# Kernel optimization log

Measured on AMD Instinct MI355X. Metric: run time of the kernel, lower is better.

Reference implementation:

```python
import jax, jax.numpy as jnp
import numpy as np

Q_NODES = 100000
S_NODES = 100000
N_EDGES = 3200000
D = 3
HIDDEN = 64
OUT_DIM = 128
STAT_DIM = 3 + 2 * D  # N_i, D_avg, D_var, Delta(D), PCA(D)


def setup_inputs() -> dict:
    key = jax.random.key(0)
    ks = jax.random.split(key, 7)
    source_pos = jax.random.normal(ks[0], (S_NODES, D), dtype=jnp.float32)
    query_pos = jax.random.normal(ks[1], (Q_NODES, D), dtype=jnp.float32)
    qi = jax.random.randint(ks[2], (N_EDGES,), 0, Q_NODES, dtype=jnp.int64)
    si = jax.random.randint(ks[3], (N_EDGES,), 0, S_NODES, dtype=jnp.int64)
    edge_index = jnp.stack([qi, si], axis=0)
    # MLP params (torch Linear default-ish scale)
    W1 = jax.random.normal(ks[4], (HIDDEN, STAT_DIM), dtype=jnp.float32) / np.sqrt(STAT_DIM)
    b1 = jnp.zeros((HIDDEN,), dtype=jnp.float32)
    W2 = jax.random.normal(ks[5], (OUT_DIM, HIDDEN), dtype=jnp.float32) / np.sqrt(HIDDEN)
    b2 = jnp.zeros((OUT_DIM,), dtype=jnp.float32)
    return {"source_pos": source_pos, "query_pos": query_pos, "edge_index": edge_index,
            "W1": W1, "b1": b1, "W2": W2, "b2": b2}


def _stat_features(source_pos, query_pos, edge_index):
    Q = query_pos.shape[0]
    qi = edge_index[0]
    si = edge_index[1]
    ones = jnp.ones(qi.shape, dtype=jnp.float32)
    counts = jax.ops.segment_sum(ones, qi, num_segments=Q)          # [Q] = N_i
    has = counts > 0
    Nc = jnp.where(has, counts, 1.0)                                 # clamp 0 -> 1

    nbr = source_pos[si]                                             # [E,D]
    qc = query_pos[qi]                                               # [E,D]
    dist = jnp.linalg.norm(nbr - qc, axis=1)                         # [E]
    D_avg = jax.ops.segment_sum(dist, qi, num_segments=Q) / Nc       # [Q]
    E_X2 = jax.ops.segment_sum(dist * dist, qi, num_segments=Q) / Nc
    D_var = jnp.maximum(E_X2 - D_avg * D_avg, 0.0)

    centroid = jax.ops.segment_sum(nbr, qi, num_segments=Q) / Nc[:, None]  # [Q,D]
    Delta = centroid - query_pos                                     # [Q,D]

    centered = nbr - centroid[qi]                                    # [E,D]
    cov_comp = centered[:, :, None] * centered[:, None, :]           # [E,D,D]
    cov = jax.ops.segment_sum(cov_comp, qi, num_segments=Q) / Nc[:, None, None]

    eig = jnp.linalg.eigvalsh(cov)[:, ::-1]                          # descending [Q,D]
    PCA = jnp.where(has[:, None], eig, 0.0)

    feats = jnp.concatenate([counts[:, None], D_avg[:, None], D_var[:, None], Delta, PCA], axis=1)
    feats = jnp.where(has[:, None], feats, 0.0)

    mean = feats.mean(axis=0, keepdims=True)
    std = jnp.std(feats, axis=0, ddof=1, keepdims=True)              # torch std is unbiased
    std = jnp.where(std < 1e-6, 1.0, std)
    return (feats - mean) / std


def reference(source_pos, query_pos, edge_index, W1, b1, W2, b2):
    feats = _stat_features(source_pos, query_pos, edge_index)        # [Q, 9]
    h = jax.nn.relu(feats @ W1.T + b1)
    return h @ W2.T + b2                                             # [Q, OUT_DIM]
```

## Files before the change

### kernel.cpp

```cpp
#include <hip/hip_runtime.h>
#include <math.h>

#define Q_NODES 100000
#define S_NODES 100000
#define N_EDGES 3200000
#define HIDDEN 64
#define OUT_DIM 128

#define QPB   128
#define NB    782
#define CAPB  4608
#define TILE  4096
#define NT4   (N_EDGES / 4)

#define F_CURSOR_OFF 0
#define F_NORM_OFF   3200
#define F_PSUM_OFF   3328
#define F_PSUMSQ_OFF 31488
#define F_FEATS_OFF  59648
#define F_SP4_OFF    3659648
#define F_SLOTS_OFF  5259648
#define F_ZERO_BYTES 3200
#define F_WS_NEED    (5259648ull + (unsigned long long)(NB * CAPB + 1) * 4)

#define B_ACC_OFF    0
#define B_STATS_OFF  4800000
#define B_NORM_OFF   4800144
#define B_FEATS_OFF  4800224
#define B_ZERO_BYTES 4800144

__device__ __forceinline__ void atomAddF(float* p, float v) {
#if defined(__gfx950__) || defined(__gfx942__) || defined(__gfx90a__)
    unsafeAtomicAdd(p, v);
#else
    atomicAdd(p, v);
#endif
}


__device__ __forceinline__ void eig3_sym(
        float a00, float a01, float a02, float a11, float a12, float a22,
        float& e1, float& e2, float& e3) {
    float p1 = a01 * a01 + a02 * a02 + a12 * a12;
    float qm = (a00 + a11 + a22) * (1.0f / 3.0f);
    float b00 = a00 - qm, b11 = a11 - qm, b22 = a22 - qm;
    float p2 = b00 * b00 + b11 * b11 + b22 * b22 + 2.0f * p1;
    if (p2 <= 1e-24f) {
        e1 = qm; e2 = qm; e3 = qm;
    } else {
        float p = sqrtf(p2 * (1.0f / 6.0f));
        float invp = 1.0f / p;
        float c00 = b00 * invp, c11 = b11 * invp, c22 = b22 * invp;
        float c01 = a01 * invp, c02 = a02 * invp, c12 = a12 * invp;
        float detB = c00 * (c11 * c22 - c12 * c12)
                   - c01 * (c01 * c22 - c12 * c02)
                   + c02 * (c01 * c12 - c11 * c02);
        float r = 0.5f * detB;
        r = fminf(fmaxf(r, -1.0f), 1.0f);
        float phi = acosf(r) * (1.0f / 3.0f);
        e1 = qm + 2.0f * p * cosf(phi);
        e3 = qm + 2.0f * p * cosf(phi + 2.0943951023931953f);
        e2 = 3.0f * qm - e1 - e3;
    }
}

__device__ __forceinline__ void sums_to_feats(
        const float* s, float qx, float qy, float qz, float* f) {
    float n = s[0];
#pragma unroll
    for (int k = 0; k < 9; ++k) f[k] = 0.0f;
    if (n > 0.0f) {
        float inv = 1.0f / n;
        float Davg = s[1] * inv;
        float Dvar = fmaxf(s[2] * inv - Davg * Davg, 0.0f);
        float cx = s[3] * inv, cy = s[4] * inv, cz = s[5] * inv;
        float a00 = fmaxf(s[6] * inv - cx * cx, 0.0f);
        float a01 = s[7] * inv - cx * cy;
        float a02 = s[8] * inv - cx * cz;
        float a11 = fmaxf(s[9] * inv - cy * cy, 0.0f);
        float a12 = s[10] * inv - cy * cz;
        float a22 = fmaxf(s[11] * inv - cz * cz, 0.0f);
        float e1, e2, e3;
        eig3_sym(a00, a01, a02, a11, a12, a22, e1, e2, e3);
        f[0] = n; f[1] = Davg; f[2] = Dvar;
        f[3] = cx - qx; f[4] = cy - qy; f[5] = cz - qz;
        f[6] = e1; f[7] = e2; f[8] = e3;
    }
}


__global__ __launch_bounds__(512, 4) void partition_kernel(
        const int* __restrict__ edge,
        const float* __restrict__ sp,
        float4* __restrict__ sp4,
        int* __restrict__ cursor,
        unsigned int* __restrict__ slots) {
    __shared__ unsigned int s_rec[TILE];
    __shared__ int s_posh[TILE];
    __shared__ int s_cur[NB];
    __shared__ int s_off[NB];
    __shared__ int s_wsum[8];

    int tid = threadIdx.x;
    int lane = tid & 63, wv = tid >> 6;
    int tileStart = blockIdx.x * TILE;
    int tileCount = N_EDGES - tileStart;
    if (tileCount > TILE) tileCount = TILE;

    {
        int i = blockIdx.x * 512 + tid;
        if (i < S_NODES)
            sp4[i] = make_float4(sp[3 * i], sp[3 * i + 1], sp[3 * i + 2], 0.0f);
    }

    for (int b = tid; b < NB; b += 512) s_posh[b] = 0;
    __syncthreads();

    const int4* eq4 = (const int4*)edge;
    const int4* es4 = (const int4*)(edge + N_EDGES);
    int base4 = blockIdx.x * (TILE / 4);
    int4 q4[2], s4[2];
    bool v[2];
#pragma unroll
    for (int j = 0; j < 2; ++j) {
        int i4 = base4 + tid + j * 512;
        v[j] = i4 < NT4;
        int ic = v[j] ? i4 : 0;
        q4[j] = eq4[ic];
        s4[j] = es4[ic];
        if (v[j]) {
            atomicAdd(&s_posh[q4[j].x >> 7], 1);
            atomicAdd(&s_posh[q4[j].y >> 7], 1);
            atomicAdd(&s_posh[q4[j].z >> 7], 1);
            atomicAdd(&s_posh[q4[j].w >> 7], 1);
        }
    }
    __syncthreads();

    int local[4], tsum = 0;
#pragma unroll
    for (int j = 0; j < 4; ++j) {
        int idx = 4 * tid + j;
        local[j] = (idx < NB) ? s_posh[idx] : 0;
        tsum += local[j];
    }
    int inc = tsum;
#pragma unroll
    for (int off = 1; off < 64; off <<= 1) {
        int t = __shfl_up(inc, off);
        if (lane >= off) inc += t;
    }
    if (lane == 63) s_wsum[wv] = inc;
    __syncthreads();
    int wbase = 0;
    for (int w = 0; w < wv; ++w) wbase += s_wsum[w];
    int run = wbase + inc - tsum;
#pragma unroll
    for (int j = 0; j < 4; ++j) {
        int idx = 4 * tid + j;
        if (idx < NB) s_cur[idx] = run;
        run += local[j];
    }
    __syncthreads();

    for (int b = tid; b < NB; b += 512) {
        int c = s_posh[b];
        int base = c ? atomicAdd(&cursor[b], c) : 0;
        s_off[b] = b * CAPB + base - s_cur[b];
    }
    __syncthreads();

#pragma unroll
    for (int j = 0; j < 2; ++j) {
        if (v[j]) {
            int qs[4] = { q4[j].x, q4[j].y, q4[j].z, q4[j].w };
            int ss[4] = { s4[j].x, s4[j].y, s4[j].z, s4[j].w };
#pragma unroll
            for (int m = 0; m < 4; ++m) {
                int bkt = qs[m] >> 7;
                int idx = atomicAdd(&s_cur[bkt], 1);
                int gpos = idx + s_off[bkt];
                if (gpos >= (bkt + 1) * CAPB) gpos = NB * CAPB;
                s_rec[idx] = ((unsigned)(qs[m] & (QPB - 1)) << 17) | (unsigned)ss[m];
                s_posh[idx] = gpos;
            }
        }
    }
    __syncthreads();

    for (int i = tid; i < tileCount; i += 512)
        slots[s_posh[i]] = s_rec[i];
}

__global__ __launch_bounds__(512) void bucket_kernel(
        const int* __restrict__ cursor,
        const unsigned int* __restrict__ slots,
        const float4* __restrict__ sp4,
        const float* __restrict__ qp,
        float* __restrict__ feats,
        float* __restrict__ psum,
        float* __restrict__ psumsq) {
    __shared__ unsigned int s_sorted[CAPB];
    __shared__ float qtile[QPB * 3];
    __shared__ int s_cnt[QPB], s_start[QPB], s_cur[QPB];
    __shared__ float s_part[4][QPB][13];
    __shared__ float s_red1[8][9], s_red2[8][9];

    int tid = threadIdx.x;
    int b = blockIdx.x;
    int cnt = cursor[b];
    if (cnt > CAPB) cnt = CAPB;

    if (tid < QPB) s_cnt[tid] = 0;
    for (int i = tid; i < QPB * 3; i += 512) {
        int g = b * QPB * 3 + i;
        qtile[i] = (g < Q_NODES * 3) ? qp[g] : 0.0f;
    }
    __syncthreads();

    const unsigned int* bslots = slots + b * CAPB;
    for (int i = tid; i < cnt; i += 512)
        atomicAdd(&s_cnt[bslots[i] >> 17], 1);
    __syncthreads();

    if (tid < 64) {
        int a0 = s_cnt[tid], a1 = s_cnt[64 + tid];
        int i0 = a0, i1 = a1;
#pragma unroll
        for (int off = 1; off < 64; off <<= 1) {
            int t0 = __shfl_up(i0, off); if (tid >= off) i0 += t0;
            int t1 = __shfl_up(i1, off); if (tid >= off) i1 += t1;
        }
        int tot0 = __shfl(i0, 63);
        s_start[tid] = i0 - a0;              s_cur[tid] = i0 - a0;
        s_start[64 + tid] = i1 - a1 + tot0;  s_cur[64 + tid] = i1 - a1 + tot0;
    }
    __syncthreads();

    for (int i = tid; i < cnt; i += 512) {
        unsigned rec = bslots[i];
        int pos = atomicAdd(&s_cur[rec >> 17], 1);
        s_sorted[pos] = rec;
    }
    __syncthreads();

    {
        int q = tid & (QPB - 1);
        int sub = tid >> 7;
        float qx = qtile[3 * q + 0], qy = qtile[3 * q + 1], qz = qtile[3 * q + 2];
        float s[12];
#pragma unroll
        for (int k = 0; k < 12; ++k) s[k] = 0.0f;
        int st = s_start[q], deg = s_cnt[q];
        for (int j = sub; j < deg; j += 4) {
            unsigned rec = s_sorted[st + j];
            float4 sv = sp4[rec & 0x1FFFF];
            float dx = sv.x - qx, dy = sv.y - qy, dz = sv.z - qz;
            float d2 = dx * dx + dy * dy + dz * dz;
            s[0] += 1.0f;
            s[1] += sqrtf(d2);
            s[2] += d2;
            s[3] += sv.x; s[4] += sv.y; s[5] += sv.z;
            s[6] += sv.x * sv.x; s[7] += sv.x * sv.y; s[8] += sv.x * sv.z;
            s[9] += sv.y * sv.y; s[10] += sv.y * sv.z; s[11] += sv.z * sv.z;
        }
#pragma unroll
        for (int k = 0; k < 12; ++k) s_part[sub][q][k] = s[k];
    }
    __syncthreads();

    float f[9];
#pragma unroll
    for (int k = 0; k < 9; ++k) f[k] = 0.0f;
    int q = b * QPB + (tid & (QPB - 1));
    if (tid < QPB && q < Q_NODES) {
        float qx = qtile[3 * tid + 0], qy = qtile[3 * tid + 1], qz = qtile[3 * tid + 2];
        float s[12];
#pragma unroll
        for (int k = 0; k < 12; ++k)
            s[k] = ((s_part[0][tid][k] + s_part[1][tid][k])
                  + (s_part[2][tid][k] + s_part[3][tid][k]));
        sums_to_feats(s, qx, qy, qz, f);
#pragma unroll
        for (int k = 0; k < 9; ++k) feats[k * Q_NODES + q] = f[k];
    }

    int lane = tid & 63, wv = tid >> 6;
#pragma unroll
    for (int k = 0; k < 9; ++k) {
        float s1 = f[k];
        float s2 = f[k] * f[k];
#pragma unroll
        for (int off = 32; off > 0; off >>= 1) {
            s1 += __shfl_down(s1, off);
            s2 += __shfl_down(s2, off);
        }
        if (lane == 0) { s_red1[wv][k] = s1; s_red2[wv][k] = s2; }
    }
    __syncthreads();
    if (tid < 9) {
        float t1 = 0.0f, t2 = 0.0f;
#pragma unroll
        for (int w = 0; w < 8; ++w) { t1 += s_red1[w][tid]; t2 += s_red2[w][tid]; }
        psum[tid * NB + b]   = t1;
        psumsq[tid * NB + b] = t2;
    }
}

__global__ __launch_bounds__(576) void stats_reduce_kernel(
        const float* __restrict__ psum,
        const float* __restrict__ psumsq,
        float* __restrict__ norm) {
    int k = threadIdx.x >> 6, lane = threadIdx.x & 63;
    if (k >= 9) return;
    double a1 = 0.0, a2 = 0.0;
    for (int b = lane; b < NB; b += 64) {
        a1 += (double)psum[k * NB + b];
        a2 += (double)psumsq[k * NB + b];
    }
#pragma unroll
    for (int off = 32; off > 0; off >>= 1) {
        a1 += __shfl_down(a1, off);
        a2 += __shfl_down(a2, off);
    }
    if (lane == 0) {
        double S = a1, S2 = a2;
        double mean = S / (double)Q_NODES;
        double var = (S2 - S * S / (double)Q_NODES) / (double)(Q_NODES - 1);
        if (var < 0.0) var = 0.0;
        double sd = sqrt(var);
        if (sd < 1e-6) sd = 1.0;
        norm[k] = (float)mean;
        norm[9 + k] = (float)(1.0 / sd);
    }
}


__global__ __launch_bounds__(256, 3) void mlp_kernel(
        const float* __restrict__ feats,
        const float* __restrict__ norm,
        const float* __restrict__ W1, const float* __restrict__ b1,
        const float* __restrict__ W2, const float* __restrict__ b2,
        float* __restrict__ out) {
    __shared__ float sW1[576];
    __shared__ float sB1[64];
    __shared__ float sB2[128];
    __shared__ float sNorm[18];
    __shared__ float w2t[64 * 64];
    __shared__ float ht[64 * 128];

    int tid = threadIdx.x;
    int blk_q = blockIdx.x;

    for (int i = tid; i < 576; i += 256) sW1[i] = W1[i];
    if (tid < 64) sB1[tid] = b1[tid];
    if (tid < 128) sB2[tid] = b2[tid];
    if (tid < 18) sNorm[tid] = norm[tid];

    {
        int o = tid & 63, kc = (tid >> 6) * 16;
#pragma unroll
        for (int j = 0; j < 16; ++j) {
            int k = kc + j;
            w2t[k * 64 + o] = W2[o * 64 + k];
        }
    }
    __syncthreads();

    {
        int q = tid & 127, half = tid >> 7;
        int qg = blk_q * 128 + q;
        int qc = qg < Q_NODES ? qg : Q_NODES - 1;
        float f[9];
#pragma unroll
        for (int k = 0; k < 9; ++k)
            f[k] = (feats[k * Q_NODES + qc] - sNorm[k]) * sNorm[9 + k];
#pragma unroll 4
        for (int j = 0; j < 32; ++j) {
            int ko = half * 32 + j;
            float a = sB1[ko];
#pragma unroll
            for (int kf = 0; kf < 9; ++kf) a = fmaf(f[kf], sW1[ko * 9 + kf], a);
            ht[ko * 128 + q] = fmaxf(a, 0.0f);
        }
    }
    __syncthreads();

    int qt = tid >> 4, ot = tid & 15;
    int q0 = qt * 8, o0 = ot * 4;

#pragma unroll 1
    for (int pass = 0; pass < 2; ++pass) {
        int oh = pass * 64;
        if (pass) {
            __syncthreads();
            int o = tid & 63, kc = (tid >> 6) * 16;
#pragma unroll
            for (int j = 0; j < 16; ++j) {
                int k = kc + j;
                w2t[k * 64 + o] = W2[(oh + o) * 64 + k];
            }
            __syncthreads();
        }

        float acc[8][4];
#pragma unroll
        for (int i = 0; i < 8; ++i)
#pragma unroll
            for (int j = 0; j < 4; ++j) acc[i][j] = 0.0f;

#pragma unroll 4
        for (int k = 0; k < 64; ++k) {
            float4 h0 = *(const float4*)&ht[k * 128 + q0];
            float4 h1 = *(const float4*)&ht[k * 128 + q0 + 4];
            float4 w  = *(const float4*)&w2t[k * 64 + o0];
            float hh[8] = { h0.x, h0.y, h0.z, h0.w, h1.x, h1.y, h1.z, h1.w };
#pragma unroll
            for (int i = 0; i < 8; ++i) {
                acc[i][0] = fmaf(hh[i], w.x, acc[i][0]);
                acc[i][1] = fmaf(hh[i], w.y, acc[i][1]);
                acc[i][2] = fmaf(hh[i], w.z, acc[i][2]);
                acc[i][3] = fmaf(hh[i], w.w, acc[i][3]);
            }
        }

        float4 bb = *(const float4*)&sB2[oh + o0];
#pragma unroll
        for (int i = 0; i < 8; ++i) {
            int qg = blk_q * 128 + q0 + i;
            if (qg < Q_NODES) {
                float4 vv = make_float4(acc[i][0] + bb.x, acc[i][1] + bb.y,
                                        acc[i][2] + bb.z, acc[i][3] + bb.w);
                *(float4*)(out + (size_t)qg * 128 + oh + o0) = vv;
            }
        }
    }
}


__global__ __launch_bounds__(256) void edge_kernel(
        const int* __restrict__ edge,
        const float* __restrict__ sp,
        const float* __restrict__ qp,
        float* __restrict__ acc) {
    int e = blockIdx.x * 256 + threadIdx.x;
    if (e >= N_EDGES) return;
    int q = edge[e];
    int s = edge[N_EDGES + e];
    float sx = sp[3 * s + 0], sy = sp[3 * s + 1], sz = sp[3 * s + 2];
    float qx = qp[3 * q + 0], qy = qp[3 * q + 1], qz = qp[3 * q + 2];
    float dx = sx - qx, dy = sy - qy, dz = sz - qz;
    float d2 = dx * dx + dy * dy + dz * dz;
    atomAddF(acc + 0 * Q_NODES + q, 1.0f);
    atomAddF(acc + 1 * Q_NODES + q, sqrtf(d2));
    atomAddF(acc + 2 * Q_NODES + q, d2);
    atomAddF(acc + 3 * Q_NODES + q, sx);
    atomAddF(acc + 4 * Q_NODES + q, sy);
    atomAddF(acc + 5 * Q_NODES + q, sz);
    atomAddF(acc + 6 * Q_NODES + q, sx * sx);
    atomAddF(acc + 7 * Q_NODES + q, sx * sy);
    atomAddF(acc + 8 * Q_NODES + q, sx * sz);
    atomAddF(acc + 9 * Q_NODES + q, sy * sy);
    atomAddF(acc + 10 * Q_NODES + q, sy * sz);
    atomAddF(acc + 11 * Q_NODES + q, sz * sz);
}

__global__ __launch_bounds__(256) void finalize_kernel(
        const float* __restrict__ acc,
        const float* __restrict__ qp,
        float* __restrict__ feats,
        double* __restrict__ stats) {
    int q = blockIdx.x * 256 + threadIdx.x;
    float f[9];
#pragma unroll
    for (int k = 0; k < 9; ++k) f[k] = 0.0f;
    if (q < Q_NODES) {
        float s[12];
#pragma unroll
        for (int k = 0; k < 12; ++k) s[k] = acc[k * Q_NODES + q];
        float qx = qp[3 * q + 0], qy = qp[3 * q + 1], qz = qp[3 * q + 2];
        sums_to_feats(s, qx, qy, qz, f);
#pragma unroll
        for (int k = 0; k < 9; ++k) feats[k * Q_NODES + q] = f[k];
    }
    int lane = threadIdx.x & 63;
#pragma unroll
    for (int k = 0; k < 9; ++k) {
        float s1 = f[k];
        float s2 = f[k] * f[k];
#pragma unroll
        for (int off = 32; off > 0; off >>= 1) {
            s1 += __shfl_down(s1, off);
            s2 += __shfl_down(s2, off);
        }
        if (lane == 0) {
            atomicAdd(&stats[k], (double)s1);
            atomicAdd(&stats[9 + k], (double)s2);
        }
    }
}

__global__ void stats_kernel(const double* __restrict__ stats,
                             float* __restrict__ norm) {
    int k = threadIdx.x;
    if (k < 9) {
        double S = stats[k], S2 = stats[9 + k];
        double mean = S / (double)Q_NODES;
        double var = (S2 - S * S / (double)Q_NODES) / (double)(Q_NODES - 1);
        if (var < 0.0) var = 0.0;
        double sd = sqrt(var);
        if (sd < 1e-6) sd = 1.0;
        norm[k] = (float)mean;
        norm[9 + k] = (float)(1.0 / sd);
    }
}


extern "C" void kernel_launch(void* const* d_in, const int* in_sizes, int n_in,
                              void* d_out, int out_size, void* d_ws, size_t ws_size,
                              hipStream_t stream) {
    const float* sp   = (const float*)d_in[0];
    const float* qp   = (const float*)d_in[1];
    const int*   edge = (const int*)d_in[2];
    const float* W1   = (const float*)d_in[3];
    const float* b1   = (const float*)d_in[4];
    const float* W2   = (const float*)d_in[5];
    const float* b2   = (const float*)d_in[6];
    float* out = (float*)d_out;
    char* ws = (char*)d_ws;

    if (ws_size >= F_WS_NEED) {
        int*          cursor = (int*)(ws + F_CURSOR_OFF);
        float*        norm   = (float*)(ws + F_NORM_OFF);
        float*        psum   = (float*)(ws + F_PSUM_OFF);
        float*        psumsq = (float*)(ws + F_PSUMSQ_OFF);
        float*        feats  = (float*)(ws + F_FEATS_OFF);
        float4*       sp4    = (float4*)(ws + F_SP4_OFF);
        unsigned int* slots  = (unsigned int*)(ws + F_SLOTS_OFF);

        hipMemsetAsync(ws, 0, F_ZERO_BYTES, stream);
        partition_kernel<<<(N_EDGES + TILE - 1) / TILE, 512, 0, stream>>>(
            edge, sp, sp4, cursor, slots);
        bucket_kernel<<<NB, 512, 0, stream>>>(cursor, slots, sp4, qp, feats, psum, psumsq);
        stats_reduce_kernel<<<1, 576, 0, stream>>>(psum, psumsq, norm);
        mlp_kernel<<<NB, 256, 0, stream>>>(feats, norm, W1, b1, W2, b2, out);
    } else {
        float*  acc   = (float*)(ws + B_ACC_OFF);
        double* stats = (double*)(ws + B_STATS_OFF);
        float*  norm  = (float*)(ws + B_NORM_OFF);
        float*  feats = (float*)(ws + B_FEATS_OFF);

        hipMemsetAsync(ws, 0, B_ZERO_BYTES, stream);
        edge_kernel<<<N_EDGES / 256, 256, 0, stream>>>(edge, sp, qp, acc);
        finalize_kernel<<<(Q_NODES + 255) / 256, 256, 0, stream>>>(acc, qp, feats, stats);
        stats_kernel<<<1, 64, 0, stream>>>(stats, norm);
        mlp_kernel<<<NB, 256, 0, stream>>>(feats, norm, W1, b1, W2, b2, out);
    }
}
```

Baseline: 193.1 us.

## Replace bucket counting sort with LDS atomics, fuse stats reduce, widen MLP

The per-bucket counting sort in LDS is removed. Each edge record now adds its 12 statistics straight into one of four replicated shared-memory accumulators using float atomics. The stats reduction is folded into the bucket kernel with a last-block-done counter, which drops one launch. Per-bucket cursors are padded to separate cache lines to cut atomic contention. The MLP now uses 512-thread blocks that stage features and the whole transposed W2 in LDS in a single pass. The trade-off is heavy LDS atomic traffic and nondeterministic summation order, in exchange for less sorting work and fewer launches.

```diff
diff --git a/kernel.cpp b/kernel.cpp
--- a/kernel.cpp
+++ b/kernel.cpp
@@ -12,16 +12,18 @@
 #define CAPB  4608
 #define TILE  4096
 #define NT4   (N_EDGES / 4)
+#define CSTR  16
 
 #define F_CURSOR_OFF 0
-#define F_NORM_OFF   3200
-#define F_PSUM_OFF   3328
-#define F_PSUMSQ_OFF 31488
-#define F_FEATS_OFF  59648
-#define F_SP4_OFF    3659648
-#define F_SLOTS_OFF  5259648
-#define F_ZERO_BYTES 3200
-#define F_WS_NEED    (5259648ull + (unsigned long long)(NB * CAPB + 1) * 4)
+#define F_DONE_OFF   50048
+#define F_NORM_OFF   50112
+#define F_PSUM_OFF   50240
+#define F_PSUMSQ_OFF 78400
+#define F_FEATS_OFF  106560
+#define F_SP4_OFF    3706560
+#define F_SLOTS_OFF  5306560
+#define F_ZERO_BYTES 50052
+#define F_WS_NEED    (5306560ull + (unsigned long long)(NB * CAPB + 1) * 4)
 
 #define B_ACC_OFF    0
 #define B_STATS_OFF  4800000
@@ -165,7 +167,7 @@
 
     for (int b = tid; b < NB; b += 512) {
         int c = s_posh[b];
-        int base = c ? atomicAdd(&cursor[b], c) : 0;
+        int base = c ? atomicAdd(&cursor[b * CSTR], c) : 0;
         s_off[b] = b * CAPB + base - s_cur[b];
     }
     __syncthreads();
@@ -192,80 +194,59 @@
         slots[s_posh[i]] = s_rec[i];
 }
 
-__global__ __launch_bounds__(512) void bucket_kernel(
+__global__ __launch_bounds__(512, 4) void bucket_kernel(
         const int* __restrict__ cursor,
         const unsigned int* __restrict__ slots,
         const float4* __restrict__ sp4,
         const float* __restrict__ qp,
         float* __restrict__ feats,
         float* __restrict__ psum,
-        float* __restrict__ psumsq) {
-    __shared__ unsigned int s_sorted[CAPB];
+        float* __restrict__ psumsq,
+        int* __restrict__ done,
+        float* __restrict__ norm) {
     __shared__ float qtile[QPB * 3];
-    __shared__ int s_cnt[QPB], s_start[QPB], s_cur[QPB];
     __shared__ float s_part[4][QPB][13];
     __shared__ float s_red1[8][9], s_red2[8][9];
+    __shared__ int s_last;
 
     int tid = threadIdx.x;
     int b = blockIdx.x;
-    int cnt = cursor[b];
+    int cnt = cursor[b * CSTR];
     if (cnt > CAPB) cnt = CAPB;
 
-    if (tid < QPB) s_cnt[tid] = 0;
     for (int i = tid; i < QPB * 3; i += 512) {
         int g = b * QPB * 3 + i;
         qtile[i] = (g < Q_NODES * 3) ? qp[g] : 0.0f;
     }
+    {
+        float* z = &s_part[0][0][0];
+        for (int i = tid; i < 4 * QPB * 13; i += 512) z[i] = 0.0f;
+    }
     __syncthreads();
 
     const unsigned int* bslots = slots + b * CAPB;
-    for (int i = tid; i < cnt; i += 512)
-        atomicAdd(&s_cnt[bslots[i] >> 17], 1);
-    __syncthreads();
-
-    if (tid < 64) {
-        int a0 = s_cnt[tid], a1 = s_cnt[64 + tid];
-        int i0 = a0, i1 = a1;
-#pragma unroll
-        for (int off = 1; off < 64; off <<= 1) {
-            int t0 = __shfl_up(i0, off); if (tid >= off) i0 += t0;
-            int t1 = __shfl_up(i1, off); if (tid >= off) i1 += t1;
-        }
-        int tot0 = __shfl(i0, 63);
-        s_start[tid] = i0 - a0;              s_cur[tid] = i0 - a0;
-        s_start[64 + tid] = i1 - a1 + tot0;  s_cur[64 + tid] = i1 - a1 + tot0;
-    }
-    __syncthreads();
-
+    int lane = tid & 63, wv = tid >> 6;
+    float* rep = &s_part[wv & 3][0][0];
     for (int i = tid; i < cnt; i += 512) {
         unsigned rec = bslots[i];
-        int pos = atomicAdd(&s_cur[rec >> 17], 1);
-        s_sorted[pos] = rec;
-    }
-    __syncthreads();
-
-    {
-        int q = tid & (QPB - 1);
-        int sub = tid >> 7;
+        int q = rec >> 17;
+        float4 sv = sp4[rec & 0x1FFFF];
         float qx = qtile[3 * q + 0], qy = qtile[3 * q + 1], qz = qtile[3 * q + 2];
-        float s[12];
-#pragma unroll
-        for (int k = 0; k < 12; ++k) s[k] = 0.0f;
-        int st = s_start[q], deg = s_cnt[q];
-        for (int j = sub; j < deg; j += 4) {
-            unsigned rec = s_sorted[st + j];
-            float4 sv = sp4[rec & 0x1FFFF];
-            float dx = sv.x - qx, dy = sv.y - qy, dz = sv.z - qz;
-            float d2 = dx * dx + dy * dy + dz * dz;
-            s[0] += 1.0f;
-            s[1] += sqrtf(d2);
-            s[2] += d2;
-            s[3] += sv.x; s[4] += sv.y; s[5] += sv.z;
-            s[6] += sv.x * sv.x; s[7] += sv.x * sv.y; s[8] += sv.x * sv.z;
-            s[9] += sv.y * sv.y; s[10] += sv.y * sv.z; s[11] += sv.z * sv.z;
-        }
-#pragma unroll
-        for (int k = 0; k < 12; ++k) s_part[sub][q][k] = s[k];
+        float dx = sv.x - qx, dy = sv.y - qy, dz = sv.z - qz;
+        float d2 = dx * dx + dy * dy + dz * dz;
+        float* pr = rep + q * 13;
+        atomicAdd(pr + 0, 1.0f);
+        atomicAdd(pr + 1, sqrtf(d2));
+        atomicAdd(pr + 2, d2);
+        atomicAdd(pr + 3, sv.x);
+        atomicAdd(pr + 4, sv.y);
+        atomicAdd(pr + 5, sv.z);
+        atomicAdd(pr + 6, sv.x * sv.x);
+        atomicAdd(pr + 7, sv.x * sv.y);
+        atomicAdd(pr + 8, sv.x * sv.z);
+        atomicAdd(pr + 9, sv.y * sv.y);
+        atomicAdd(pr + 10, sv.y * sv.z);
+        atomicAdd(pr + 11, sv.z * sv.z);
     }
     __syncthreads();
 
@@ -285,7 +266,6 @@
         for (int k = 0; k < 9; ++k) feats[k * Q_NODES + q] = f[k];
     }
 
-    int lane = tid & 63, wv = tid >> 6;
 #pragma unroll
     for (int k = 0; k < 9; ++k) {
         float s1 = f[k];
@@ -305,38 +285,40 @@
         psum[tid * NB + b]   = t1;
         psumsq[tid * NB + b] = t2;
     }
-}
-
-__global__ __launch_bounds__(576) void stats_reduce_kernel(
-        const float* __restrict__ psum,
-        const float* __restrict__ psumsq,
-        float* __restrict__ norm) {
-    int k = threadIdx.x >> 6, lane = threadIdx.x & 63;
-    if (k >= 9) return;
-    double a1 = 0.0, a2 = 0.0;
-    for (int b = lane; b < NB; b += 64) {
-        a1 += (double)psum[k * NB + b];
-        a2 += (double)psumsq[k * NB + b];
-    }
-#pragma unroll
-    for (int off = 32; off > 0; off >>= 1) {
-        a1 += __shfl_down(a1, off);
-        a2 += __shfl_down(a2, off);
-    }
-    if (lane == 0) {
-        double S = a1, S2 = a2;
-        double mean = S / (double)Q_NODES;
-        double var = (S2 - S * S / (double)Q_NODES) / (double)(Q_NODES - 1);
-        if (var < 0.0) var = 0.0;
-        double sd = sqrt(var);
-        if (sd < 1e-6) sd = 1.0;
-        norm[k] = (float)mean;
-        norm[9 + k] = (float)(1.0 / sd);
-    }
-}
-
-
-__global__ __launch_bounds__(256, 3) void mlp_kernel(
+    __threadfence();
+    __syncthreads();
+    if (tid == 0) s_last = (atomicAdd(done, 1) == NB - 1);
+    __syncthreads();
+    if (s_last) {
+        __threadfence();
+        int k = tid >> 5, l32 = tid & 31;
+        if (k < 9) {
+            double a1 = 0.0, a2 = 0.0;
+            for (int bb = l32; bb < NB; bb += 32) {
+                a1 += (double)psum[k * NB + bb];
+                a2 += (double)psumsq[k * NB + bb];
+            }
+#pragma unroll
+            for (int off = 16; off > 0; off >>= 1) {
+                a1 += __shfl_down(a1, off);
+                a2 += __shfl_down(a2, off);
+            }
+            if (l32 == 0) {
+                double S = a1, S2 = a2;
+                double mean = S / (double)Q_NODES;
+                double var = (S2 - S * S / (double)Q_NODES) / (double)(Q_NODES - 1);
+                if (var < 0.0) var = 0.0;
+                double sd = sqrt(var);
+                if (sd < 1e-6) sd = 1.0;
+                norm[k] = (float)mean;
+                norm[9 + k] = (float)(1.0 / sd);
+            }
+        }
+    }
+}
+
+
+__global__ __launch_bounds__(512, 2) void mlp_kernel(
         const float* __restrict__ feats,
         const float* __restrict__ norm,
         const float* __restrict__ W1, const float* __restrict__ b1,
@@ -346,93 +328,87 @@
     __shared__ float sB1[64];
     __shared__ float sB2[128];
     __shared__ float sNorm[18];
-    __shared__ float w2t[64 * 64];
+    __shared__ float sfeat[9 * 128];
+    __shared__ float w2t[64 * 128];
     __shared__ float ht[64 * 128];
 
     int tid = threadIdx.x;
     int blk_q = blockIdx.x;
 
-    for (int i = tid; i < 576; i += 256) sW1[i] = W1[i];
+    for (int i = tid; i < 9 * 128; i += 512) {
+        int k = i >> 7, qq = i & 127;
+        int qg = blk_q * 128 + qq;
+        if (qg >= Q_NODES) qg = Q_NODES - 1;
+        sfeat[i] = feats[k * Q_NODES + qg];
+    }
+
+    {
+        int o = tid & 127, kb = (tid >> 7) * 16;
+        const float4* w2v = (const float4*)(W2 + o * 64 + kb);
+#pragma unroll
+        for (int j = 0; j < 4; ++j) {
+            float4 w = w2v[j];
+            int k = kb + j * 4;
+            w2t[(k + 0) * 128 + o] = w.x;
+            w2t[(k + 1) * 128 + o] = w.y;
+            w2t[(k + 2) * 128 + o] = w.z;
+            w2t[(k + 3) * 128 + o] = w.w;
+        }
+    }
+    for (int i = tid; i < 576; i += 512) sW1[i] = W1[i];
     if (tid < 64) sB1[tid] = b1[tid];
     if (tid < 128) sB2[tid] = b2[tid];
     if (tid < 18) sNorm[tid] = norm[tid];
+    __syncthreads();
 
     {
-        int o = tid & 63, kc = (tid >> 6) * 16;
-#pragma unroll
+        int qq = tid & 127, quarter = tid >> 7;
+        float f[9];
+#pragma unroll
+        for (int k = 0; k < 9; ++k)
+            f[k] = (sfeat[k * 128 + qq] - sNorm[k]) * sNorm[9 + k];
+#pragma unroll 4
         for (int j = 0; j < 16; ++j) {
-            int k = kc + j;
-            w2t[k * 64 + o] = W2[o * 64 + k];
-        }
-    }
-    __syncthreads();
-
-    {
-        int q = tid & 127, half = tid >> 7;
-        int qg = blk_q * 128 + q;
-        int qc = qg < Q_NODES ? qg : Q_NODES - 1;
-        float f[9];
-#pragma unroll
-        for (int k = 0; k < 9; ++k)
-            f[k] = (feats[k * Q_NODES + qc] - sNorm[k]) * sNorm[9 + k];
+            int ko = quarter * 16 + j;
+            float a = sB1[ko];
+#pragma unroll
+            for (int kf = 0; kf < 9; ++kf) a = fmaf(f[kf], sW1[ko * 9 + kf], a);
+            ht[ko * 128 + qq] = fmaxf(a, 0.0f);
+        }
+    }
+    __syncthreads();
+
+    int qt = tid >> 5, ot = tid & 31;
+    int q0 = qt * 8, o0 = ot * 4;
+    float acc[8][4];
+#pragma unroll
+    for (int i = 0; i < 8; ++i)
+#pragma unroll
+        for (int j = 0; j < 4; ++j) acc[i][j] = 0.0f;
+
 #pragma unroll 4
-        for (int j = 0; j < 32; ++j) {
-            int ko = half * 32 + j;
-            float a = sB1[ko];
-#pragma unroll
-            for (int kf = 0; kf < 9; ++kf) a = fmaf(f[kf], sW1[ko * 9 + kf], a);
-            ht[ko * 128 + q] = fmaxf(a, 0.0f);
-        }
-    }
-    __syncthreads();
-
-    int qt = tid >> 4, ot = tid & 15;
-    int q0 = qt * 8, o0 = ot * 4;
-
-#pragma unroll 1
-    for (int pass = 0; pass < 2; ++pass) {
-        int oh = pass * 64;
-        if (pass) {
-            __syncthreads();
-            int o = tid & 63, kc = (tid >> 6) * 16;
-#pragma unroll
-            for (int j = 0; j < 16; ++j) {
-                int k = kc + j;
-                w2t[k * 64 + o] = W2[(oh + o) * 64 + k];
-            }
-            __syncthreads();
-        }
-
-        float acc[8][4];
-#pragma unroll
-        for (int i = 0; i < 8; ++i)
-#pragma unroll
-            for (int j = 0; j < 4; ++j) acc[i][j] = 0.0f;
-
-#pragma unroll 4
-        for (int k = 0; k < 64; ++k) {
-            float4 h0 = *(const float4*)&ht[k * 128 + q0];
-            float4 h1 = *(const float4*)&ht[k * 128 + q0 + 4];
-            float4 w  = *(const float4*)&w2t[k * 64 + o0];
-            float hh[8] = { h0.x, h0.y, h0.z, h0.w, h1.x, h1.y, h1.z, h1.w };
-#pragma unroll
-            for (int i = 0; i < 8; ++i) {
-                acc[i][0] = fmaf(hh[i], w.x, acc[i][0]);
-                acc[i][1] = fmaf(hh[i], w.y, acc[i][1]);
-                acc[i][2] = fmaf(hh[i], w.z, acc[i][2]);
-                acc[i][3] = fmaf(hh[i], w.w, acc[i][3]);
-            }
-        }
-
-        float4 bb = *(const float4*)&sB2[oh + o0];
+    for (int k = 0; k < 64; ++k) {
+        float4 h0 = *(const float4*)&ht[k * 128 + q0];
+        float4 h1 = *(const float4*)&ht[k * 128 + q0 + 4];
+        float4 w  = *(const float4*)&w2t[k * 128 + o0];
+        float hh[8] = { h0.x, h0.y, h0.z, h0.w, h1.x, h1.y, h1.z, h1.w };
 #pragma unroll
         for (int i = 0; i < 8; ++i) {
-            int qg = blk_q * 128 + q0 + i;
-            if (qg < Q_NODES) {
-                float4 vv = make_float4(acc[i][0] + bb.x, acc[i][1] + bb.y,
-                                        acc[i][2] + bb.z, acc[i][3] + bb.w);
-                *(float4*)(out + (size_t)qg * 128 + oh + o0) = vv;
-            }
+            acc[i][0] = fmaf(hh[i], w.x, acc[i][0]);
+            acc[i][1] = fmaf(hh[i], w.y, acc[i][1]);
+            acc[i][2] = fmaf(hh[i], w.z, acc[i][2]);
+            acc[i][3] = fmaf(hh[i], w.w, acc[i][3]);
+        }
+    }
+
+    float4 bb = *(const float4*)&sB2[o0];
+#pragma unroll
+    for (int i = 0; i < 8; ++i) {
+        int qg = blk_q * 128 + q0 + i;
+        if (qg < Q_NODES) {
+            float4 vv = make_float4(acc[i][0] + bb.x, acc[i][1] + bb.y,
+                                    acc[i][2] + bb.z, acc[i][3] + bb.w);
+            *(float4*)(out + (size_t)qg * 128 + o0) = vv;
         }
     }
 }
@@ -531,6 +507,7 @@
 
     if (ws_size >= F_WS_NEED) {
         int*          cursor = (int*)(ws + F_CURSOR_OFF);
+        int*          done   = (int*)(ws + F_DONE_OFF);
         float*        norm   = (float*)(ws + F_NORM_OFF);
         float*        psum   = (float*)(ws + F_PSUM_OFF);
         float*        psumsq = (float*)(ws + F_PSUMSQ_OFF);
@@ -541,9 +518,9 @@
         hipMemsetAsync(ws, 0, F_ZERO_BYTES, stream);
         partition_kernel<<<(N_EDGES + TILE - 1) / TILE, 512, 0, stream>>>(
             edge, sp, sp4, cursor, slots);
-        bucket_kernel<<<NB, 512, 0, stream>>>(cursor, slots, sp4, qp, feats, psum, psumsq);
-        stats_reduce_kernel<<<1, 576, 0, stream>>>(psum, psumsq, norm);
-        mlp_kernel<<<NB, 256, 0, stream>>>(feats, norm, W1, b1, W2, b2, out);
+        bucket_kernel<<<NB, 512, 0, stream>>>(
+            cursor, slots, sp4, qp, feats, psum, psumsq, done, norm);
+        mlp_kernel<<<NB, 512, 0, stream>>>(feats, norm, W1, b1, W2, b2, out);
     } else {
         float*  acc   = (float*)(ws + B_ACC_OFF);
         double* stats = (double*)(ws + B_STATS_OFF);
@@ -554,6 +531,6 @@
         edge_kernel<<<N_EDGES / 256, 256, 0, stream>>>(edge, sp, qp, acc);
         finalize_kernel<<<(Q_NODES + 255) / 256, 256, 0, stream>>>(acc, qp, feats, stats);
         stats_kernel<<<1, 64, 0, stream>>>(stats, norm);
-        mlp_kernel<<<NB, 256, 0, stream>>>(feats, norm, W1, b1, W2, b2, out);
-    }
-}
+        mlp_kernel<<<NB, 512, 0, stream>>>(feats, norm, W1, b1, W2, b2, out);
+    }
+}
```

After: 479.1 us. +148.1%, slower.
